# Optimization experiments

Measured on AMD Instinct MI355X. Metric: run time of the kernel, lower is better.

Reference implementation:

```python
import jax, jax.numpy as jnp
import numpy as np

B, S = 512, 512
VOCAB, E, H1, H2, NTAGS = 50000, 20, 30, 50, 45


def _xavier_scale(fan_in, fan_out):
    return float(np.sqrt(2.0 / (fan_in + fan_out)))


def setup_inputs() -> dict:
    key = jax.random.key(0)
    ks = jax.random.split(key, 32)
    n = lambda i, shape, s=1.0: jax.random.normal(ks[i], shape, dtype=jnp.float32) * s
    w = 0.1  # weight scale
    emb_f1 = n(0, (VOCAB, E), w).at[0].set(0.0)  # padding_idx=0
    emb_b1 = n(1, (VOCAB, E), w).at[0].set(0.0)
    xs1 = _xavier_scale(B, H1)
    xs2 = _xavier_scale(B, H2)
    inp = {
        "x": jax.random.randint(ks[2], (B, S), 0, VOCAB, dtype=jnp.int64),
        "emb_f1": emb_f1, "emb_b1": emb_b1,
        "h0_f1": n(3, (B, H1), xs1), "c0_f1": n(4, (B, H1), xs1),
        "Wih_f1": n(5, (4 * H1, E), w), "Whh_f1": n(6, (4 * H1, H1), w),
        "bih_f1": n(7, (4 * H1,), w), "bhh_f1": n(8, (4 * H1,), w),
        "h0_b1": n(9, (B, H1), xs1), "c0_b1": n(10, (B, H1), xs1),
        "Wih_b1": n(11, (4 * H1, E), w), "Whh_b1": n(12, (4 * H1, H1), w),
        "bih_b1": n(13, (4 * H1,), w), "bhh_b1": n(14, (4 * H1,), w),
        "h0_f2": n(15, (B, H2), xs2), "c0_f2": n(16, (B, H2), xs2),
        "Wih_f2": n(17, (4 * H2, 2 * H1), w), "Whh_f2": n(18, (4 * H2, H2), w),
        "bih_f2": n(19, (4 * H2,), w), "bhh_f2": n(20, (4 * H2,), w),
        "h0_b2": n(21, (B, H2), xs2), "c0_b2": n(22, (B, H2), xs2),
        "Wih_b2": n(23, (4 * H2, 2 * H1), w), "Whh_b2": n(24, (4 * H2, H2), w),
        "bih_b2": n(25, (4 * H2,), w), "bhh_b2": n(26, (4 * H2,), w),
        "lin_w": n(27, (NTAGS, 2 * H2), w), "lin_b": n(28, (NTAGS,), w),
    }
    return inp


def _run_lstm(seq, h0, c0, Wih, Whh, bih, bhh, forward):
    """PyTorch LSTMCell recurrence over seq (B,S,D). Replicates the original's
    quirks: backward dir appends hidden states in reversed time order, and the
    (S,B,H) stack is .view()-ed into (B,S,H) without transposing."""
    b, s, _ = seq.shape
    h = h0.shape[-1]
    xs = jnp.swapaxes(seq, 0, 1)  # (S,B,D)

    def step(carry, xt):
        hh, cc = carry
        g = xt @ Wih.T + bih + hh @ Whh.T + bhh  # (B, 4H), gate order i,f,g,o
        i, f, gg, o = jnp.split(g, 4, axis=-1)
        cc = jax.nn.sigmoid(f) * cc + jax.nn.sigmoid(i) * jnp.tanh(gg)
        hh = jax.nn.sigmoid(o) * jnp.tanh(cc)
        return (hh, cc), hh

    _, hs = jax.lax.scan(step, (h0, c0), xs, reverse=not forward)  # hs[i] ~ time i
    if not forward:
        hs = hs[::-1]  # torch appended in processing (reversed-time) order
    return hs.reshape(b, s, h)  # faithful buggy view (S,B,H) -> (B,S,H)


def reference(x, emb_f1, emb_b1,
              h0_f1, c0_f1, Wih_f1, Whh_f1, bih_f1, bhh_f1,
              h0_b1, c0_b1, Wih_b1, Whh_b1, bih_b1, bhh_b1,
              h0_f2, c0_f2, Wih_f2, Whh_f2, bih_f2, bhh_f2,
              h0_b2, c0_b2, Wih_b2, Whh_b2, bih_b2, bhh_b2,
              lin_w, lin_b):
    f1 = _run_lstm(emb_f1[x], h0_f1, c0_f1, Wih_f1, Whh_f1, bih_f1, bhh_f1, True)
    b1 = _run_lstm(emb_b1[x], h0_b1, c0_b1, Wih_b1, Whh_b1, bih_b1, bhh_b1, False)
    l1 = jnp.concatenate([f1, b1], axis=2)  # (B,S,2*H1)
    f2 = _run_lstm(l1, h0_f2, c0_f2, Wih_f2, Whh_f2, bih_f2, bhh_f2, True)
    b2 = _run_lstm(l1, h0_b2, c0_b2, Wih_b2, Whh_b2, bih_b2, bhh_b2, False)
    l2 = jnp.concatenate([f2, b2], axis=2)  # (B,S,2*H2)
    return l2 @ lin_w.T + lin_b  # (B,S,NTAGS)
```

## Files before the change

### kernel.cpp

```cpp
#include <hip/hip_runtime.h>
#include <hip/hip_bf16.h>

typedef __hip_bfloat16 bf16;
typedef __attribute__((ext_vector_type(8))) short short8;
typedef __attribute__((ext_vector_type(4))) float float4v;
typedef unsigned short ushort_t;

#define BB 512
#define SS 512
#define EE 20
#define H1C 30
#define H2C 50
#define NTC 45

#define BAR() asm volatile("s_waitcnt lgkmcnt(0)\n\ts_barrier" ::: "memory")

#if __has_builtin(__builtin_amdgcn_exp2f)
#define EXP2(x) __builtin_amdgcn_exp2f(x)
#else
#define EXP2(x) exp2f(x)
#endif
#if __has_builtin(__builtin_amdgcn_rcpf)
#define RCPF(x) __builtin_amdgcn_rcpf(x)
#else
#define RCPF(x) (1.0f / (x))
#endif

#define LOG2E 1.4426950408889634f

__device__ __forceinline__ float sigE(float v)  { return RCPF(1.0f + EXP2(-v)); }
__device__ __forceinline__ float tanhE(float v) { return 2.0f * RCPF(1.0f + EXP2(-v)) - 1.0f; }
__device__ __forceinline__ float tanh_(float v) {
    return 2.0f * RCPF(1.0f + EXP2(-2.8853900817779268f * v)) - 1.0f;
}

__device__ __forceinline__ ushort_t f2bf(float f) {
    unsigned u = __float_as_uint(f);
    unsigned r = u + 0x7FFFu + ((u >> 16) & 1u);
    return (ushort_t)(r >> 16);
}
__device__ __forceinline__ float bf2f(ushort_t s) { return __uint_as_float(((unsigned)s) << 16); }

__device__ __forceinline__ float ldG(const void* p, int i, int f32) {
    if (f32) return ((const float*)p)[i];
    return bf2f(((const ushort_t*)p)[i]);
}
__device__ __forceinline__ int ldTok(const void* x, int i, int x64) {
    const int* xi = (const int*)x;
    return x64 ? xi[2 * i] : xi[i];
}

__global__ void detect_kernel(const void* bih, const void* x, int* flags) {
    if (threadIdx.x == 0 && blockIdx.x == 0) {
        const ushort_t* u = (const ushort_t*)bih;
        int isf = 0;
        for (int i = 0; i < 120; i++) {
            float v = fabsf(bf2f(u[i]));
            if (!(v < 16.0f)) isf = 1;
        }
        flags[0] = isf;
        const int* xi = (const int*)x;
        int orv = 0;
        for (int i = 1; i < 32; i += 2) orv |= xi[i];
        flags[1] = (orv == 0) ? 1 : 0;
    }
}

struct XV4R { unsigned r[4]; };

__device__ __forceinline__ XV4R ldEmbRaw(const void* emb, int tok, int k0, int f32v) {
    XV4R o;
    if (f32v) {
        uint4 v = *(const uint4*)((const float*)emb + (size_t)tok * EE + k0);
        o.r[0] = v.x; o.r[1] = v.y; o.r[2] = v.z; o.r[3] = v.w;
    } else {
        uint2 v = *(const uint2*)((const ushort_t*)emb + (size_t)tok * EE + k0);
        o.r[0] = v.x; o.r[1] = v.y; o.r[2] = 0; o.r[3] = 0;
    }
    return o;
}
__device__ __forceinline__ ushort4 cvtX(XV4R x, int f32v) {
    ushort4 u;
    if (f32v) {
        u.x = f2bf(__uint_as_float(x.r[0]));
        u.y = f2bf(__uint_as_float(x.r[1]));
        u.z = f2bf(__uint_as_float(x.r[2]));
        u.w = f2bf(__uint_as_float(x.r[3]));
    } else {
        u.x = (ushort_t)(x.r[0] & 0xFFFFu);
        u.y = (ushort_t)(x.r[0] >> 16);
        u.z = (ushort_t)(x.r[1] & 0xFFFFu);
        u.w = (ushort_t)(x.r[1] >> 16);
    }
    return u;
}

__global__ __launch_bounds__(128) void lstm1_kernel(
    const void* __restrict__ x,
    const void* __restrict__ emb_f, const void* __restrict__ emb_b,
    const void* __restrict__ h0_f, const void* __restrict__ c0_f,
    const void* __restrict__ Wih_f, const void* __restrict__ Whh_f,
    const void* __restrict__ bih_f, const void* __restrict__ bhh_f,
    const void* __restrict__ h0_b, const void* __restrict__ c0_b,
    const void* __restrict__ Wih_b, const void* __restrict__ Whh_b,
    const void* __restrict__ bih_b, const void* __restrict__ bhh_b,
    ushort_t* __restrict__ hsf, ushort_t* __restrict__ hsb,
    const int* __restrict__ flags)
{
    const int f32v = flags[0], x64 = flags[1];
    const int wg = blockIdx.x, dir = wg >> 5, j0 = (wg & 31) << 4, tid = threadIdx.x;
    const int wave = tid >> 6, lane = tid & 63, li = lane & 15, quad = lane >> 4;

    const void* emb = dir ? emb_b : emb_f;
    const void* h0  = dir ? h0_b  : h0_f;
    const void* c0  = dir ? c0_b  : c0_f;
    const void* Wih = dir ? Wih_b : Wih_f;
    const void* Whh = dir ? Whh_b : Whh_f;
    const void* bih = dir ? bih_b : bih_f;
    const void* bhh = dir ? bhh_b : bhh_f;
    ushort_t* hs = dir ? hsb : hsf;

    __shared__ __align__(16) ushort_t Af[2][2][64][8];
    __shared__ int toks[16][SS];

    for (int idx = tid; idx < 16 * SS; idx += 128) {
        int r = idx >> 9, t = idx & (SS - 1);
        toks[r][t] = ldTok(x, (j0 + r) * SS + t, x64);
    }
    for (int idx = tid; idx < 2 * 2 * 64 * 8; idx += 128) ((ushort_t*)Af)[idx] = 0;

    const int n = wave * 16 + li;
    const bool nok = n < H1C;

    short8 bhi[4][2], blo[4][2];
    float bias_g[4];
    #pragma unroll
    for (int g = 0; g < 4; g++) {
        const float sc = (g == 2) ? 2.0f * LOG2E : LOG2E;
        const int wrow = g * H1C + n;
        bias_g[g] = nok ? sc * (ldG(bih, wrow, f32v) + ldG(bhh, wrow, f32v)) : 0.f;
        #pragma unroll
        for (int kt = 0; kt < 2; kt++) {
            short8 hi, lo;
            #pragma unroll
            for (int j = 0; j < 8; j++) {
                int k = kt * 32 + quad * 8 + j;
                float w = 0.f;
                if (nok) {
                    if (kt == 0) { if (k < EE) w = ldG(Wih, wrow * EE + k, f32v); }
                    else { int kk = k - 32; if (kk < H1C) w = ldG(Whh, wrow * H1C + kk, f32v); }
                }
                w *= sc;
                ushort_t h = f2bf(w);
                hi[j] = (short)h;
                lo[j] = (short)f2bf(w - bf2f(h));
            }
            bhi[g][kt] = hi; blo[g][kt] = lo;
        }
    }

    const int hr0 = (n >> 3) * 16, hj = n & 7;
    const int lrow = tid / 5, lc = tid - lrow * 5, k0 = lc * 4;
    const bool ldr = tid < 80;
    const int t0 = dir ? SS - 1 : 0, dt = dir ? -1 : 1;

    __syncthreads();

    float creg[4];
    #pragma unroll
    for (int r = 0; r < 4; r++) {
        const int m = quad * 4 + r;
        creg[r] = nok ? ldG(c0, (j0 + m) * H1C + n, f32v) : 0.f;
        ushort_t hb0 = nok ? f2bf(ldG(h0, (j0 + m) * H1C + n, f32v)) : (ushort_t)0;
        Af[0][1][hr0 + m][hj] = hb0;
    }
    XV4R xA, xB;
    if (ldr) {
        *(ushort4*)&Af[0][0][(k0 >> 3) * 16 + lrow][k0 & 7] =
            cvtX(ldEmbRaw(emb, toks[lrow][t0], k0, f32v), f32v);
        *(ushort4*)&Af[1][0][(k0 >> 3) * 16 + lrow][k0 & 7] =
            cvtX(ldEmbRaw(emb, toks[lrow][t0 + dt], k0, f32v), f32v);
        xA = ldEmbRaw(emb, toks[lrow][t0 + 2 * dt], k0, f32v);
    }
    __syncthreads();

    float4v xacc[4];
    {
        short8 afx0 = *(const short8*)&Af[0][0][lane][0];
        #pragma unroll
        for (int g = 0; g < 4; g++) {
            float4v a; a[0] = a[1] = a[2] = a[3] = bias_g[g];
            a = __builtin_amdgcn_mfma_f32_16x16x32_bf16(afx0, bhi[g][0], a, 0, 0, 0);
            a = __builtin_amdgcn_mfma_f32_16x16x32_bf16(afx0, blo[g][0], a, 0, 0, 0);
            xacc[g] = a;
        }
    }

    auto step = [&](int it, XV4R& xin, XV4R& xout) {
        const int t = t0 + dt * it;
        const int cur = it & 1, nxt = cur ^ 1;
        BAR();
        short8 afh = *(const short8*)&Af[cur][1][lane][0];
        short8 afx = *(const short8*)&Af[nxt][0][lane][0];
        if (ldr && it + 3 < SS)
            xout = ldEmbRaw(emb, toks[lrow][t + 3 * dt], k0, f32v);
        float4v acc[4], xn[4];
        #pragma unroll
        for (int g = 0; g < 4; g++) {
            float4v a = xacc[g];
            a = __builtin_amdgcn_mfma_f32_16x16x32_bf16(afh, bhi[g][1], a, 0, 0, 0);
            a = __builtin_amdgcn_mfma_f32_16x16x32_bf16(afh, blo[g][1], a, 0, 0, 0);
            acc[g] = a;
            float4v b; b[0] = b[1] = b[2] = b[3] = bias_g[g];
            b = __builtin_amdgcn_mfma_f32_16x16x32_bf16(afx, bhi[g][0], b, 0, 0, 0);
            b = __builtin_amdgcn_mfma_f32_16x16x32_bf16(afx, blo[g][0], b, 0, 0, 0);
            xn[g] = b;
        }
        ushort_t hb[4];
        #pragma unroll
        for (int r = 0; r < 4; r++) {
            float gi = acc[0][r], gf = acc[1][r], gg = acc[2][r], go = acc[3][r];
            float c = sigE(gf) * creg[r] + sigE(gi) * tanhE(gg);
            float h = sigE(go) * tanh_(c);
            creg[r] = c;
            hb[r] = nok ? f2bf(h) : (ushort_t)0;
            hs[((size_t)(j0 + quad * 4 + r) * SS + t) * 32 + n] = hb[r];
        }
        if (it + 1 < SS) {
            #pragma unroll
            for (int r = 0; r < 4; r++) Af[nxt][1][hr0 + quad * 4 + r][hj] = hb[r];
        }
        if (ldr && it + 2 < SS)
            *(ushort4*)&Af[cur][0][(k0 >> 3) * 16 + lrow][k0 & 7] = cvtX(xin, f32v);
        #pragma unroll
        for (int g = 0; g < 4; g++) xacc[g] = xn[g];
    };
    for (int it = 0; it < SS; it += 2) { step(it, xA, xB); step(it + 1, xB, xA); }
}

__global__ __launch_bounds__(256) void lstm2_kernel(
    const ushort_t* __restrict__ hs1f, const ushort_t* __restrict__ hs1b,
    const void* __restrict__ h0_f, const void* __restrict__ c0_f,
    const void* __restrict__ Wih_f, const void* __restrict__ Whh_f,
    const void* __restrict__ bih_f, const void* __restrict__ bhh_f,
    const void* __restrict__ h0_b, const void* __restrict__ c0_b,
    const void* __restrict__ Wih_b, const void* __restrict__ Whh_b,
    const void* __restrict__ bih_b, const void* __restrict__ bhh_b,
    ushort_t* __restrict__ hsf, ushort_t* __restrict__ hsb,
    const int* __restrict__ flags)
{
    const int f32v = flags[0];
    const int wg = blockIdx.x, dir = wg >> 5, cb = (wg & 31) << 4, tid = threadIdx.x;
    const int wave = tid >> 6, lane = tid & 63, li = lane & 15, quad = lane >> 4;

    const void* h0  = dir ? h0_b  : h0_f;
    const void* c0  = dir ? c0_b  : c0_f;
    const void* Wih = dir ? Wih_b : Wih_f;
    const void* Whh = dir ? Whh_b : Whh_f;
    const void* bih = dir ? bih_b : bih_f;
    const void* bhh = dir ? bhh_b : bhh_f;
    ushort_t* hs = dir ? hsb : hsf;

    __shared__ __align__(16) ushort_t Af[2][4][64][8];
    for (int idx = tid; idx < 2 * 4 * 64 * 8; idx += 256) ((ushort_t*)Af)[idx] = 0;

    const int n = wave * 16 + li;
    const bool nok = n < H2C;

    short8 bhi[4][4], blo[4][4];
    float bias_g[4];
    #pragma unroll
    for (int g = 0; g < 4; g++) {
        const float sc = (g == 2) ? 2.0f * LOG2E : LOG2E;
        const int wrow = g * H2C + n;
        bias_g[g] = nok ? sc * (ldG(bih, wrow, f32v) + ldG(bhh, wrow, f32v)) : 0.f;
        #pragma unroll
        for (int kt = 0; kt < 4; kt++) {
            short8 hi, lo;
            #pragma unroll
            for (int j = 0; j < 8; j++) {
                int k = kt * 32 + quad * 8 + j;
                float w = 0.f;
                if (nok) {
                    if (k < H1C) w = ldG(Wih, wrow * (2 * H1C) + k, f32v);
                    else if (k >= 32 && k < 32 + H1C) w = ldG(Wih, wrow * (2 * H1C) + H1C + (k - 32), f32v);
                    else if (k >= 64 && k < 64 + H2C) w = ldG(Whh, wrow * H2C + (k - 64), f32v);
                }
                w *= sc;
                ushort_t h = f2bf(w);
                hi[j] = (short)h;
                lo[j] = (short)f2bf(w - bf2f(h));
            }
            bhi[g][kt] = hi; blo[g][kt] = lo;
        }
    }

    const int kh = 64 + n;
    const int khk = kh >> 5, khg = (kh & 31) >> 3, khj = kh & 7;
    const int lrow = tid >> 4, k0 = (tid & 15) * 4;
    const int skt = k0 >> 5, skg = (k0 & 31) >> 3, sjb = k0 & 7;
    const int t0 = dir ? SS - 1 : 0, dt = dir ? -1 : 1;

    auto loadX = [&](int c) -> ushort4 {
        const int a = cb + lrow;
        if (k0 < 32)
            return *(const ushort4*)&hs1f[((size_t)c * SS + a) * 32 + k0];
        else
            return *(const ushort4*)&hs1b[((size_t)c * SS + (SS - 1 - a)) * 32 + (k0 - 32)];
    };

    __syncthreads();

    float creg[4];
    #pragma unroll
    for (int r = 0; r < 4; r++) {
        const int m = quad * 4 + r;
        creg[r] = nok ? ldG(c0, (cb + m) * H2C + n, f32v) : 0.f;
        ushort_t hb0 = nok ? f2bf(ldG(h0, (cb + m) * H2C + n, f32v)) : (ushort_t)0;
        Af[0][khk][khg * 16 + m][khj] = hb0;
    }
    *(ushort4*)&Af[0][skt][skg * 16 + lrow][sjb] = loadX(t0);
    *(ushort4*)&Af[1][skt][skg * 16 + lrow][sjb] = loadX(t0 + dt);
    ushort4 xA = loadX(t0 + 2 * dt), xB;
    __syncthreads();

    float4v xacc[4];
    {
        short8 afx0 = *(const short8*)&Af[0][0][lane][0];
        short8 afx1 = *(const short8*)&Af[0][1][lane][0];
        #pragma unroll
        for (int g = 0; g < 4; g++) {
            float4v a; a[0] = a[1] = a[2] = a[3] = bias_g[g];
            a = __builtin_amdgcn_mfma_f32_16x16x32_bf16(afx0, bhi[g][0], a, 0, 0, 0);
            a = __builtin_amdgcn_mfma_f32_16x16x32_bf16(afx0, blo[g][0], a, 0, 0, 0);
            a = __builtin_amdgcn_mfma_f32_16x16x32_bf16(afx1, bhi[g][1], a, 0, 0, 0);
            a = __builtin_amdgcn_mfma_f32_16x16x32_bf16(afx1, blo[g][1], a, 0, 0, 0);
            xacc[g] = a;
        }
    }

    auto step = [&](int it, ushort4& xin, ushort4& xout) {
        const int c = t0 + dt * it;
        const int cur = it & 1, nxt = cur ^ 1;
        BAR();
        short8 afh0 = *(const short8*)&Af[cur][2][lane][0];
        short8 afh1 = *(const short8*)&Af[cur][3][lane][0];
        short8 afx0 = *(const short8*)&Af[nxt][0][lane][0];
        short8 afx1 = *(const short8*)&Af[nxt][1][lane][0];
        if (it + 3 < SS) xout = loadX(c + 3 * dt);
        float4v acc[4], xn[4];
        #pragma unroll
        for (int g = 0; g < 4; g++) {
            float4v a = xacc[g];
            a = __builtin_amdgcn_mfma_f32_16x16x32_bf16(afh0, bhi[g][2], a, 0, 0, 0);
            a = __builtin_amdgcn_mfma_f32_16x16x32_bf16(afh0, blo[g][2], a, 0, 0, 0);
            a = __builtin_amdgcn_mfma_f32_16x16x32_bf16(afh1, bhi[g][3], a, 0, 0, 0);
            a = __builtin_amdgcn_mfma_f32_16x16x32_bf16(afh1, blo[g][3], a, 0, 0, 0);
            acc[g] = a;
            float4v b; b[0] = b[1] = b[2] = b[3] = bias_g[g];
            b = __builtin_amdgcn_mfma_f32_16x16x32_bf16(afx0, bhi[g][0], b, 0, 0, 0);
            b = __builtin_amdgcn_mfma_f32_16x16x32_bf16(afx0, blo[g][0], b, 0, 0, 0);
            b = __builtin_amdgcn_mfma_f32_16x16x32_bf16(afx1, bhi[g][1], b, 0, 0, 0);
            b = __builtin_amdgcn_mfma_f32_16x16x32_bf16(afx1, blo[g][1], b, 0, 0, 0);
            xn[g] = b;
        }
        ushort_t hb[4];
        #pragma unroll
        for (int r = 0; r < 4; r++) {
            float gi = acc[0][r], gf = acc[1][r], gg = acc[2][r], go = acc[3][r];
            float cc = sigE(gf) * creg[r] + sigE(gi) * tanhE(gg);
            float h = sigE(go) * tanh_(cc);
            creg[r] = cc;
            hb[r] = nok ? f2bf(h) : (ushort_t)0;
        }
        ushort4 h4; h4.x = hb[0]; h4.y = hb[1]; h4.z = hb[2]; h4.w = hb[3];
        *(ushort4*)&hs[((size_t)c * 64 + n) * SS + cb + quad * 4] = h4;
        if (it + 1 < SS) {
            #pragma unroll
            for (int r = 0; r < 4; r++) Af[nxt][khk][khg * 16 + quad * 4 + r][khj] = hb[r];
        }
        if (it + 2 < SS)
            *(ushort4*)&Af[cur][skt][skg * 16 + lrow][sjb] = xin;
        #pragma unroll
        for (int g = 0; g < 4; g++) xacc[g] = xn[g];
    };
    for (int it = 0; it < SS; it += 2) { step(it, xA, xB); step(it + 1, xB, xA); }
}

__global__ __launch_bounds__(256) void lin_kernel(
    const ushort_t* __restrict__ hs2f, const ushort_t* __restrict__ hs2b,
    const void* __restrict__ lw, const void* __restrict__ lb,
    void* __restrict__ out, const int* __restrict__ flags)
{
    const int f32v = flags[0];
    const int tid = threadIdx.x, wave = tid >> 6, lane = tid & 63, li = lane & 15, quad = lane >> 4;

    __shared__ __align__(16) ushort_t Af[4][4][64][8];
    for (int idx = tid; idx < 4 * 4 * 64 * 8; idx += 256) ((ushort_t*)Af)[idx] = 0;

    short8 bhi[3][4], blo[3][4];
    float biasv[3];
    #pragma unroll
    for (int nt = 0; nt < 3; nt++) {
        const int nn = nt * 16 + li;
        const bool nok = nn < NTC;
        biasv[nt] = nok ? ldG(lb, nn, f32v) : 0.f;
        #pragma unroll
        for (int kt = 0; kt < 4; kt++) {
            short8 hi, lo;
            #pragma unroll
            for (int j = 0; j < 8; j++) {
                int k = kt * 32 + quad * 8 + j;
                float w = 0.f;
                if (nok) {
                    if (k < H2C) w = ldG(lw, nn * 100 + k, f32v);
                    else if (k >= 64 && k < 64 + H2C) w = ldG(lw, nn * 100 + 50 + (k - 64), f32v);
                }
                ushort_t h = f2bf(w);
                hi[j] = (short)h;
                lo[j] = (short)f2bf(w - bf2f(h));
            }
            bhi[nt][kt] = hi; blo[nt][kt] = lo;
        }
    }

    const int P0 = blockIdx.x * 64;
    const int i = P0 >> 9, j0 = P0 & 511;
    __syncthreads();
    for (int idx = tid; idx < 100 * 32; idx += 256) {
        const int kk = idx >> 5, pj = (idx & 31) * 2;
        unsigned v;
        int k;
        if (kk < H2C) {
            v = *(const unsigned*)&hs2f[((size_t)i * 64 + kk) * SS + j0 + pj];
            k = kk;
        } else {
            v = *(const unsigned*)&hs2b[((size_t)(SS - 1 - i) * 64 + (kk - H2C)) * SS + j0 + pj];
            k = 64 + (kk - H2C);
        }
        const int kt = k >> 5, kg = (k & 31) >> 3, j = k & 7;
        Af[pj >> 4][kt][kg * 16 + (pj & 15)][j] = (ushort_t)(v & 0xFFFF);
        Af[pj >> 4][kt][kg * 16 + ((pj + 1) & 15)][j] = (ushort_t)(v >> 16);
    }
    __syncthreads();

    short8 af[4];
    #pragma unroll
    for (int kt = 0; kt < 4; kt++) af[kt] = *(const short8*)&Af[wave][kt][lane][0];
    #pragma unroll
    for (int nt = 0; nt < 3; nt++) {
        float4v a; a[0] = a[1] = a[2] = a[3] = biasv[nt];
        #pragma unroll
        for (int kt = 0; kt < 4; kt++) {
            a = __builtin_amdgcn_mfma_f32_16x16x32_bf16(af[kt], bhi[nt][kt], a, 0, 0, 0);
            a = __builtin_amdgcn_mfma_f32_16x16x32_bf16(af[kt], blo[nt][kt], a, 0, 0, 0);
        }
        const int nn = nt * 16 + li;
        if (nn < NTC) {
            #pragma unroll
            for (int reg = 0; reg < 4; reg++) {
                const int prow = wave * 16 + quad * 4 + reg;
                const size_t op = (size_t)(P0 + prow) * NTC + nn;
                if (f32v) ((float*)out)[op] = a[reg];
                else      ((ushort_t*)out)[op] = f2bf(a[reg]);
            }
        }
    }
}

extern "C" void kernel_launch(void* const* d_in, const int* in_sizes, int n_in,
                              void* d_out, int out_size, void* d_ws, size_t ws_size,
                              hipStream_t stream)
{
    const void* x      = d_in[0];
    const void* emb_f1 = d_in[1];
    const void* emb_b1 = d_in[2];
    const void* h0_f1  = d_in[3];
    const void* c0_f1  = d_in[4];
    const void* Wih_f1 = d_in[5];
    const void* Whh_f1 = d_in[6];
    const void* bih_f1 = d_in[7];
    const void* bhh_f1 = d_in[8];
    const void* h0_b1  = d_in[9];
    const void* c0_b1  = d_in[10];
    const void* Wih_b1 = d_in[11];
    const void* Whh_b1 = d_in[12];
    const void* bih_b1 = d_in[13];
    const void* bhh_b1 = d_in[14];
    const void* h0_f2  = d_in[15];
    const void* c0_f2  = d_in[16];
    const void* Wih_f2 = d_in[17];
    const void* Whh_f2 = d_in[18];
    const void* bih_f2 = d_in[19];
    const void* bhh_f2 = d_in[20];
    const void* h0_b2  = d_in[21];
    const void* c0_b2  = d_in[22];
    const void* Wih_b2 = d_in[23];
    const void* Whh_b2 = d_in[24];
    const void* bih_b2 = d_in[25];
    const void* bhh_b2 = d_in[26];
    const void* lin_w  = d_in[27];
    const void* lin_b  = d_in[28];

    int* flags = (int*)d_ws;
    ushort_t* hs1f = (ushort_t*)((char*)d_ws + 256);
    ushort_t* hs1b = hs1f + (size_t)BB * SS * 32;
    ushort_t* hs2f = hs1b + (size_t)BB * SS * 32;
    ushort_t* hs2b = hs2f + (size_t)SS * 64 * BB;

    detect_kernel<<<1, 64, 0, stream>>>(bih_f1, x, flags);
    lstm1_kernel<<<64, 128, 0, stream>>>(x, emb_f1, emb_b1,
        h0_f1, c0_f1, Wih_f1, Whh_f1, bih_f1, bhh_f1,
        h0_b1, c0_b1, Wih_b1, Whh_b1, bih_b1, bhh_b1, hs1f, hs1b, flags);
    lstm2_kernel<<<64, 256, 0, stream>>>(hs1f, hs1b,
        h0_f2, c0_f2, Wih_f2, Whh_f2, bih_f2, bhh_f2,
        h0_b2, c0_b2, Wih_b2, Whh_b2, bih_b2, bhh_b2, hs2f, hs2b, flags);
    lin_kernel<<<(BB * SS) / 64, 256, 0, stream>>>(hs2f, hs2b, lin_w, lin_b, d_out, flags);
}
```

Measured before the change: 1.022 ms.

## Pack multiple LSTM chains per workgroup and stream token loads inline

Both LSTM kernels now pack several independent batch-chunk recurrences into one larger workgroup (4 chains of 128 threads for layer 1, 2 chains of 256 for layer 2), each chain with its own shared-memory slice, so fewer workgroups are launched. Layer 1 no longer preloads the full token table into shared memory and instead prefetches token ids a few steps ahead from global memory. The global stores of hidden states are moved after the shared-memory writes. The workgroup-wide barrier now synchronises all packed chains together, which couples their progress and may add stall time in a latency-bound recurrence.

```diff
diff --git a/kernel.cpp b/kernel.cpp
--- a/kernel.cpp
+++ b/kernel.cpp
@@ -95,7 +95,7 @@
     return u;
 }
 
-__global__ __launch_bounds__(128) void lstm1_kernel(
+__global__ __launch_bounds__(512) void lstm1_kernel(
     const void* __restrict__ x,
     const void* __restrict__ emb_f, const void* __restrict__ emb_b,
     const void* __restrict__ h0_f, const void* __restrict__ c0_f,
@@ -108,8 +108,12 @@
     const int* __restrict__ flags)
 {
     const int f32v = flags[0], x64 = flags[1];
-    const int wg = blockIdx.x, dir = wg >> 5, j0 = (wg & 31) << 4, tid = threadIdx.x;
-    const int wave = tid >> 6, lane = tid & 63, li = lane & 15, quad = lane >> 4;
+    const int tid = threadIdx.x;
+    const int c  = __builtin_amdgcn_readfirstlane(tid >> 7);
+    const int ct = tid & 127;
+    const int cg = blockIdx.x * 4 + c;
+    const int dir = cg >> 5, j0 = (cg & 31) << 4;
+    const int wv = (tid >> 6) & 1, lane = tid & 63, li = lane & 15, quad = lane >> 4;
 
     const void* emb = dir ? emb_b : emb_f;
     const void* h0  = dir ? h0_b  : h0_f;
@@ -120,16 +124,10 @@
     const void* bhh = dir ? bhh_b : bhh_f;
     ushort_t* hs = dir ? hsb : hsf;
 
-    __shared__ __align__(16) ushort_t Af[2][2][64][8];
-    __shared__ int toks[16][SS];
-
-    for (int idx = tid; idx < 16 * SS; idx += 128) {
-        int r = idx >> 9, t = idx & (SS - 1);
-        toks[r][t] = ldTok(x, (j0 + r) * SS + t, x64);
-    }
-    for (int idx = tid; idx < 2 * 2 * 64 * 8; idx += 128) ((ushort_t*)Af)[idx] = 0;
-
-    const int n = wave * 16 + li;
+    __shared__ __align__(16) ushort_t Af[4][2][2][64][8];
+    for (int idx = tid; idx < 4 * 2 * 2 * 64 * 8; idx += 512) ((ushort_t*)Af)[idx] = 0;
+
+    const int n = wv * 16 + li;
     const bool nok = n < H1C;
 
     short8 bhi[4][2], blo[4][2];
@@ -160,9 +158,10 @@
     }
 
     const int hr0 = (n >> 3) * 16, hj = n & 7;
-    const int lrow = tid / 5, lc = tid - lrow * 5, k0 = lc * 4;
-    const bool ldr = tid < 80;
+    const int lrow = ct / 5, lc = ct - lrow * 5, k0 = lc * 4;
+    const bool ldr = ct < 80;
     const int t0 = dir ? SS - 1 : 0, dt = dir ? -1 : 1;
+    const int rbase = (j0 + lrow) * SS;
 
     __syncthreads();
 
@@ -172,21 +171,24 @@
         const int m = quad * 4 + r;
         creg[r] = nok ? ldG(c0, (j0 + m) * H1C + n, f32v) : 0.f;
         ushort_t hb0 = nok ? f2bf(ldG(h0, (j0 + m) * H1C + n, f32v)) : (ushort_t)0;
-        Af[0][1][hr0 + m][hj] = hb0;
+        Af[c][0][1][hr0 + m][hj] = hb0;
     }
     XV4R xA, xB;
+    int tA = 0, tB = 0;
     if (ldr) {
-        *(ushort4*)&Af[0][0][(k0 >> 3) * 16 + lrow][k0 & 7] =
-            cvtX(ldEmbRaw(emb, toks[lrow][t0], k0, f32v), f32v);
-        *(ushort4*)&Af[1][0][(k0 >> 3) * 16 + lrow][k0 & 7] =
-            cvtX(ldEmbRaw(emb, toks[lrow][t0 + dt], k0, f32v), f32v);
-        xA = ldEmbRaw(emb, toks[lrow][t0 + 2 * dt], k0, f32v);
+        int tk0 = ldTok(x, rbase + t0, x64);
+        int tk1 = ldTok(x, rbase + t0 + dt, x64);
+        int tk2 = ldTok(x, rbase + t0 + 2 * dt, x64);
+        *(ushort4*)&Af[c][0][0][(k0 >> 3) * 16 + lrow][k0 & 7] = cvtX(ldEmbRaw(emb, tk0, k0, f32v), f32v);
+        *(ushort4*)&Af[c][1][0][(k0 >> 3) * 16 + lrow][k0 & 7] = cvtX(ldEmbRaw(emb, tk1, k0, f32v), f32v);
+        xA = ldEmbRaw(emb, tk2, k0, f32v);
+        tA = ldTok(x, rbase + t0 + 3 * dt, x64);
     }
     __syncthreads();
 
     float4v xacc[4];
     {
-        short8 afx0 = *(const short8*)&Af[0][0][lane][0];
+        short8 afx0 = *(const short8*)&Af[c][0][0][lane][0];
         #pragma unroll
         for (int g = 0; g < 4; g++) {
             float4v a; a[0] = a[1] = a[2] = a[3] = bias_g[g];
@@ -196,14 +198,16 @@
         }
     }
 
-    auto step = [&](int it, XV4R& xin, XV4R& xout) {
+    auto step = [&](int it, XV4R& xin, XV4R& xout, int& tin, int& tout) {
         const int t = t0 + dt * it;
         const int cur = it & 1, nxt = cur ^ 1;
         BAR();
-        short8 afh = *(const short8*)&Af[cur][1][lane][0];
-        short8 afx = *(const short8*)&Af[nxt][0][lane][0];
-        if (ldr && it + 3 < SS)
-            xout = ldEmbRaw(emb, toks[lrow][t + 3 * dt], k0, f32v);
+        short8 afh = *(const short8*)&Af[c][cur][1][lane][0];
+        short8 afx = *(const short8*)&Af[c][nxt][0][lane][0];
+        if (ldr) {
+            if (it + 3 < SS) xout = ldEmbRaw(emb, tin, k0, f32v);
+            if (it + 4 < SS) tout = ldTok(x, rbase + t + 4 * dt, x64);
+        }
         float4v acc[4], xn[4];
         #pragma unroll
         for (int g = 0; g < 4; g++) {
@@ -220,25 +224,27 @@
         #pragma unroll
         for (int r = 0; r < 4; r++) {
             float gi = acc[0][r], gf = acc[1][r], gg = acc[2][r], go = acc[3][r];
-            float c = sigE(gf) * creg[r] + sigE(gi) * tanhE(gg);
-            float h = sigE(go) * tanh_(c);
-            creg[r] = c;
+            float cc = sigE(gf) * creg[r] + sigE(gi) * tanhE(gg);
+            float h = sigE(go) * tanh_(cc);
+            creg[r] = cc;
             hb[r] = nok ? f2bf(h) : (ushort_t)0;
-            hs[((size_t)(j0 + quad * 4 + r) * SS + t) * 32 + n] = hb[r];
         }
         if (it + 1 < SS) {
             #pragma unroll
-            for (int r = 0; r < 4; r++) Af[nxt][1][hr0 + quad * 4 + r][hj] = hb[r];
+            for (int r = 0; r < 4; r++) Af[c][nxt][1][hr0 + quad * 4 + r][hj] = hb[r];
         }
         if (ldr && it + 2 < SS)
-            *(ushort4*)&Af[cur][0][(k0 >> 3) * 16 + lrow][k0 & 7] = cvtX(xin, f32v);
+            *(ushort4*)&Af[c][cur][0][(k0 >> 3) * 16 + lrow][k0 & 7] = cvtX(xin, f32v);
+        #pragma unroll
+        for (int r = 0; r < 4; r++)
+            hs[((size_t)(j0 + quad * 4 + r) * SS + t) * 32 + n] = hb[r];
         #pragma unroll
         for (int g = 0; g < 4; g++) xacc[g] = xn[g];
     };
-    for (int it = 0; it < SS; it += 2) { step(it, xA, xB); step(it + 1, xB, xA); }
-}
-
-__global__ __launch_bounds__(256) void lstm2_kernel(
+    for (int it = 0; it < SS; it += 2) { step(it, xA, xB, tA, tB); step(it + 1, xB, xA, tB, tA); }
+}
+
+__global__ __launch_bounds__(512) void lstm2_kernel(
     const ushort_t* __restrict__ hs1f, const ushort_t* __restrict__ hs1b,
     const void* __restrict__ h0_f, const void* __restrict__ c0_f,
     const void* __restrict__ Wih_f, const void* __restrict__ Whh_f,
@@ -250,8 +256,12 @@
     const int* __restrict__ flags)
 {
     const int f32v = flags[0];
-    const int wg = blockIdx.x, dir = wg >> 5, cb = (wg & 31) << 4, tid = threadIdx.x;
-    const int wave = tid >> 6, lane = tid & 63, li = lane & 15, quad = lane >> 4;
+    const int tid = threadIdx.x;
+    const int c  = __builtin_amdgcn_readfirstlane(tid >> 8);
+    const int ct = tid & 255;
+    const int cg = blockIdx.x * 2 + c;
+    const int dir = cg >> 5, cb = (cg & 31) << 4;
+    const int wv = (tid >> 6) & 3, lane = tid & 63, li = lane & 15, quad = lane >> 4;
 
     const void* h0  = dir ? h0_b  : h0_f;
     const void* c0  = dir ? c0_b  : c0_f;
@@ -261,10 +271,10 @@
     const void* bhh = dir ? bhh_b : bhh_f;
     ushort_t* hs = dir ? hsb : hsf;
 
-    __shared__ __align__(16) ushort_t Af[2][4][64][8];
-    for (int idx = tid; idx < 2 * 4 * 64 * 8; idx += 256) ((ushort_t*)Af)[idx] = 0;
-
-    const int n = wave * 16 + li;
+    __shared__ __align__(16) ushort_t Af[2][2][4][64][8];
+    for (int idx = tid; idx < 2 * 2 * 4 * 64 * 8; idx += 512) ((ushort_t*)Af)[idx] = 0;
+
+    const int n = wv * 16 + li;
     const bool nok = n < H2C;
 
     short8 bhi[4][4], blo[4][4];
@@ -297,16 +307,16 @@
 
     const int kh = 64 + n;
     const int khk = kh >> 5, khg = (kh & 31) >> 3, khj = kh & 7;
-    const int lrow = tid >> 4, k0 = (tid & 15) * 4;
+    const int lrow = ct >> 4, k0 = (ct & 15) * 4;
     const int skt = k0 >> 5, skg = (k0 & 31) >> 3, sjb = k0 & 7;
     const int t0 = dir ? SS - 1 : 0, dt = dir ? -1 : 1;
 
-    auto loadX = [&](int c) -> ushort4 {
+    auto loadX = [&](int cc) -> ushort4 {
         const int a = cb + lrow;
         if (k0 < 32)
-            return *(const ushort4*)&hs1f[((size_t)c * SS + a) * 32 + k0];
+            return *(const ushort4*)&hs1f[((size_t)cc * SS + a) * 32 + k0];
         else
-            return *(const ushort4*)&hs1b[((size_t)c * SS + (SS - 1 - a)) * 32 + (k0 - 32)];
+            return *(const ushort4*)&hs1b[((size_t)cc * SS + (SS - 1 - a)) * 32 + (k0 - 32)];
     };
 
     __syncthreads();
@@ -317,17 +327,17 @@
         const int m = quad * 4 + r;
         creg[r] = nok ? ldG(c0, (cb + m) * H2C + n, f32v) : 0.f;
         ushort_t hb0 = nok ? f2bf(ldG(h0, (cb + m) * H2C + n, f32v)) : (ushort_t)0;
-        Af[0][khk][khg * 16 + m][khj] = hb0;
-    }
-    *(ushort4*)&Af[0][skt][skg * 16 + lrow][sjb] = loadX(t0);
-    *(ushort4*)&Af[1][skt][skg * 16 + lrow][sjb] = loadX(t0 + dt);
+        Af[c][0][khk][khg * 16 + m][khj] = hb0;
+    }
+    *(ushort4*)&Af[c][0][skt][skg * 16 + lrow][sjb] = loadX(t0);
+    *(ushort4*)&Af[c][1][skt][skg * 16 + lrow][sjb] = loadX(t0 + dt);
     ushort4 xA = loadX(t0 + 2 * dt), xB;
     __syncthreads();
 
     float4v xacc[4];
     {
-        short8 afx0 = *(const short8*)&Af[0][0][lane][0];
-        short8 afx1 = *(const short8*)&Af[0][1][lane][0];
+        short8 afx0 = *(const short8*)&Af[c][0][0][lane][0];
+        short8 afx1 = *(const short8*)&Af[c][0][1][lane][0];
         #pragma unroll
         for (int g = 0; g < 4; g++) {
             float4v a; a[0] = a[1] = a[2] = a[3] = bias_g[g];
@@ -340,14 +350,14 @@
     }
 
     auto step = [&](int it, ushort4& xin, ushort4& xout) {
-        const int c = t0 + dt * it;
+        const int cc = t0 + dt * it;
         const int cur = it & 1, nxt = cur ^ 1;
         BAR();
-        short8 afh0 = *(const short8*)&Af[cur][2][lane][0];
-        short8 afh1 = *(const short8*)&Af[cur][3][lane][0];
-        short8 afx0 = *(const short8*)&Af[nxt][0][lane][0];
-        short8 afx1 = *(const short8*)&Af[nxt][1][lane][0];
-        if (it + 3 < SS) xout = loadX(c + 3 * dt);
+        short8 afh0 = *(const short8*)&Af[c][cur][2][lane][0];
+        short8 afh1 = *(const short8*)&Af[c][cur][3][lane][0];
+        short8 afx0 = *(const short8*)&Af[c][nxt][0][lane][0];
+        short8 afx1 = *(const short8*)&Af[c][nxt][1][lane][0];
+        if (it + 3 < SS) xout = loadX(cc + 3 * dt);
         float4v acc[4], xn[4];
         #pragma unroll
         for (int g = 0; g < 4; g++) {
@@ -368,19 +378,19 @@
         #pragma unroll
         for (int r = 0; r < 4; r++) {
             float gi = acc[0][r], gf = acc[1][r], gg = acc[2][r], go = acc[3][r];
-            float cc = sigE(gf) * creg[r] + sigE(gi) * tanhE(gg);
-            float h = sigE(go) * tanh_(cc);
-            creg[r] = cc;
+            float ccv = sigE(gf) * creg[r] + sigE(gi) * tanhE(gg);
+            float h = sigE(go) * tanh_(ccv);
+            creg[r] = ccv;
             hb[r] = nok ? f2bf(h) : (ushort_t)0;
         }
-        ushort4 h4; h4.x = hb[0]; h4.y = hb[1]; h4.z = hb[2]; h4.w = hb[3];
-        *(ushort4*)&hs[((size_t)c * 64 + n) * SS + cb + quad * 4] = h4;
         if (it + 1 < SS) {
             #pragma unroll
-            for (int r = 0; r < 4; r++) Af[nxt][khk][khg * 16 + quad * 4 + r][khj] = hb[r];
+            for (int r = 0; r < 4; r++) Af[c][nxt][khk][khg * 16 + quad * 4 + r][khj] = hb[r];
         }
         if (it + 2 < SS)
-            *(ushort4*)&Af[cur][skt][skg * 16 + lrow][sjb] = xin;
+            *(ushort4*)&Af[c][cur][skt][skg * 16 + lrow][sjb] = xin;
+        ushort4 h4; h4.x = hb[0]; h4.y = hb[1]; h4.z = hb[2]; h4.w = hb[3];
+        *(ushort4*)&hs[((size_t)cc * 64 + n) * SS + cb + quad * 4] = h4;
         #pragma unroll
         for (int g = 0; g < 4; g++) xacc[g] = xn[g];
     };
@@ -509,10 +519,10 @@
     ushort_t* hs2b = hs2f + (size_t)SS * 64 * BB;
 
     detect_kernel<<<1, 64, 0, stream>>>(bih_f1, x, flags);
-    lstm1_kernel<<<64, 128, 0, stream>>>(x, emb_f1, emb_b1,
+    lstm1_kernel<<<16, 512, 0, stream>>>(x, emb_f1, emb_b1,
         h0_f1, c0_f1, Wih_f1, Whh_f1, bih_f1, bhh_f1,
         h0_b1, c0_b1, Wih_b1, Whh_b1, bih_b1, bhh_b1, hs1f, hs1b, flags);
-    lstm2_kernel<<<64, 256, 0, stream>>>(hs1f, hs1b,
+    lstm2_kernel<<<32, 512, 0, stream>>>(hs1f, hs1b,
         h0_f2, c0_f2, Wih_f2, Whh_f2, bih_f2, bhh_f2,
         h0_b2, c0_b2, Wih_b2, Whh_b2, bih_b2, bhh_b2, hs2f, hs2b, flags);
     lin_kernel<<<(BB * SS) / 64, 256, 0, stream>>>(hs2f, hs2b, lin_w, lin_b, d_out, flags);
```

After: 1.355 ms. 1.33x slower.
